# Optimization experiments

Measured on AMD Instinct MI355X. Metric: run time of the kernel, lower is better.

## Reference

```python
import jax, jax.numpy as jnp
import numpy as np

NUM_RELS = 1315
FEAT_DIM = 768
RD = 32  # rel_emb_dim
OD = 32  # out_dim
B = 65536  # entities per side
NNZ = 1048576  # nonzeros per incidence matrix (avg degree 16)
EPS = 1e-12  # torch F.normalize eps


def _normalize(x):
    n = jnp.linalg.norm(x, axis=1, keepdims=True)
    return x / jnp.maximum(n, EPS)


def _agg(rows, cols, vals, rel_emb):
    # sparse.mm(inc, rel_emb): gather rel rows, scale, scatter-add to entities -> [B, RD]
    return jax.ops.segment_sum(vals[:, None] * rel_emb[cols], rows, num_segments=B)


def _entity_emb(ri, ci, vi, ro, co, vo, feat, rel_emb, W_in, b_in, W_out, b_out, W_ent, b_ent):
    in_emb = _agg(ri, ci, vi, rel_emb) @ W_in.T + b_in
    out_emb = _agg(ro, co, vo, rel_emb) @ W_out.T + b_out
    f = jnp.concatenate([feat, in_emb, out_emb], axis=1)  # [B, FEAT+2*RD]
    return _normalize(f @ W_ent.T + b_ent)


def setup_inputs() -> dict:
    key = jax.random.key(0)
    ks = iter(jax.random.split(key, 40))
    d = {}
    for p in ("h", "pos_t", "neg_t"):
        for s in ("in", "out"):
            d[f"{p}_{s}_rows"] = jax.random.randint(next(ks), (NNZ,), 0, B, dtype=jnp.int32)
            d[f"{p}_{s}_cols"] = jax.random.randint(next(ks), (NNZ,), 0, NUM_RELS, dtype=jnp.int32)
            d[f"{p}_{s}_vals"] = jax.random.uniform(next(ks), (NNZ,), dtype=jnp.float32)
        d[f"{p}_node_feat"] = jax.random.normal(next(ks), (B, FEAT_DIM), dtype=jnp.float32)
    d["eid"] = jax.random.randint(next(ks), (B,), 0, NUM_RELS, dtype=jnp.int32)
    # learned parameters
    d["rel_emb"] = jax.random.normal(next(ks), (NUM_RELS, RD), dtype=jnp.float32) * 0.02
    d["W_in"] = jax.random.normal(next(ks), (RD, RD), dtype=jnp.float32) * 0.1
    d["b_in"] = jnp.zeros((RD,), dtype=jnp.float32)
    d["W_out"] = jax.random.normal(next(ks), (RD, RD), dtype=jnp.float32) * 0.1
    d["b_out"] = jnp.zeros((RD,), dtype=jnp.float32)
    d["W_ent"] = jax.random.normal(next(ks), (OD, FEAT_DIM + 2 * RD), dtype=jnp.float32) * 0.02
    d["b_ent"] = jnp.zeros((OD,), dtype=jnp.float32)
    d["W_rel"] = jax.random.normal(next(ks), (OD, RD), dtype=jnp.float32) * 0.1
    d["b_rel"] = jnp.zeros((OD,), dtype=jnp.float32)
    return d


def reference(h_in_rows, h_in_cols, h_in_vals, h_out_rows, h_out_cols, h_out_vals, h_node_feat,
              pos_t_in_rows, pos_t_in_cols, pos_t_in_vals, pos_t_out_rows, pos_t_out_cols, pos_t_out_vals, pos_t_node_feat,
              neg_t_in_rows, neg_t_in_cols, neg_t_in_vals, neg_t_out_rows, neg_t_out_cols, neg_t_out_vals, neg_t_node_feat,
              eid, rel_emb, W_in, b_in, W_out, b_out, W_ent, b_ent, W_rel, b_rel):
    r_emb = _normalize(rel_emb[eid] @ W_rel.T + b_rel)  # [B, OD]
    h_emb = _entity_emb(h_in_rows, h_in_cols, h_in_vals, h_out_rows, h_out_cols, h_out_vals,
                        h_node_feat, rel_emb, W_in, b_in, W_out, b_out, W_ent, b_ent)
    pos_t_emb = _entity_emb(pos_t_in_rows, pos_t_in_cols, pos_t_in_vals, pos_t_out_rows, pos_t_out_cols, pos_t_out_vals,
                            pos_t_node_feat, rel_emb, W_in, b_in, W_out, b_out, W_ent, b_ent)
    neg_t_emb = _entity_emb(neg_t_in_rows, neg_t_in_cols, neg_t_in_vals, neg_t_out_rows, neg_t_out_cols, neg_t_out_vals,
                            neg_t_node_feat, rel_emb, W_in, b_in, W_out, b_out, W_ent, b_ent)
    pos_score = jnp.linalg.norm(h_emb + r_emb - pos_t_emb, axis=1)
    neg_score = jnp.linalg.norm(h_emb + r_emb - neg_t_emb, axis=1)
    return (pos_score, neg_score)
```

## Files before the change

kernel.cpp:

```cpp
#include <hip/hip_runtime.h>
#include <math.h>

#define N_RELS 1315
#define NB 65536
#define NNZV (1 << 20)
#define FEATD 768

#define NBUK 256
#define CAP  4608
#define FPT  9

typedef float f32x4 __attribute__((ext_vector_type(4)));
typedef short s16x8 __attribute__((ext_vector_type(8)));
typedef float v2f  __attribute__((ext_vector_type(2)));

struct Mats { const int* rows[6]; const int* cols[6]; const float* vals[6]; };

__device__ __forceinline__ short f2bf(float f) {
    return __builtin_bit_cast(short, (__bf16)f);
}

__global__ void k_prep(const float* __restrict__ rel_emb,
                       const float* __restrict__ W_in, const float* __restrict__ b_in,
                       const float* __restrict__ W_out, const float* __restrict__ b_out,
                       const float* __restrict__ W_ent, const float* __restrict__ b_ent,
                       const float* __restrict__ W_rel, const float* __restrict__ b_rel,
                       float* __restrict__ Pcat, float* __restrict__ Prel,
                       float* __restrict__ bprime, unsigned* __restrict__ cursor)
{
    __shared__ float C[2][32][33];
    const int tid = threadIdx.x;
    if (cursor != nullptr && blockIdx.x < 6) {
        const int i = blockIdx.x * 256 + tid;
        cursor[i] = (unsigned)i * CAP;
    }
    for (int idx = tid; idx < 2 * 32 * 32; idx += 256) {
        int d = idx >> 10, o = (idx >> 5) & 31, t = idx & 31;
        const float* W  = d ? W_out : W_in;
        const float* we = W_ent + o * 832 + 768 + d * 32;
        float s = 0.f;
        #pragma unroll
        for (int j = 0; j < 32; ++j) s += we[j] * W[j * 32 + t];
        C[d][o][t] = s;
    }
    __syncthreads();

    const int row8 = blockIdx.x * 8 + (tid >> 5);
    const int o = tid & 31;
    if (row8 < 2 * N_RELS) {
        const int d = (row8 >= N_RELS) ? 1 : 0;
        const int r = row8 - d * N_RELS;
        const float* re = rel_emb + r * 32;
        float s = 0.f;
        #pragma unroll
        for (int t = 0; t < 32; ++t) s += re[t] * C[d][o][t];
        Pcat[row8 * 32 + o] = s;
    } else if (row8 < 3 * N_RELS) {
        const int r = row8 - 2 * N_RELS;
        const float* re = rel_emb + r * 32;
        float s = b_rel[o];
        #pragma unroll
        for (int j = 0; j < 32; ++j) s += W_rel[o * 32 + j] * re[j];
        float sq = s * s;
        #pragma unroll
        for (int m = 16; m; m >>= 1) sq += __shfl_xor(sq, m);
        Prel[r * 32 + o] = s / fmaxf(sqrtf(sq), 1e-12f);
    }
    if (blockIdx.x == 0 && tid < 32) {
        float s = b_ent[tid];
        #pragma unroll
        for (int j = 0; j < 32; ++j)
            s += b_in[j] * W_ent[tid * 832 + 768 + j] + b_out[j] * W_ent[tid * 832 + 800 + j];
        bprime[tid] = s;
    }
}

__global__ void k_wfrag(const float* __restrict__ W_ent, s16x8* __restrict__ wsB)
{
    const int t = blockIdx.x * 256 + threadIdx.x;
    if (t >= 24 * 2 * 64) return;
    const int kk = t >> 7, rem = t & 127, nt = rem >> 6, l = rem & 63;
    const int col = nt * 16 + (l & 15);
    const int k0  = kk * 32 + ((l >> 4) << 3);
    const float* w = W_ent + col * 832 + k0;
    s16x8 v;
    #pragma unroll
    for (int e = 0; e < 8; ++e) v[e] = f2bf(w[e]);
    wsB[t] = v;
}

__global__ __launch_bounds__(512) void k_bin(Mats m, uint2* __restrict__ bins,
                                             unsigned* __restrict__ cursor)
{
    __shared__ uint2 stage[4096];
    __shared__ int hist[256], sc[256], ofs[256];
    __shared__ unsigned gbase[256];
    const int bi    = blockIdx.x;
    const int mm    = bi >> 8;
    const int chunk = bi & 255;
    const int tid   = threadIdx.x;
    const int* __restrict__ R = m.rows[mm];
    const int* __restrict__ C = m.cols[mm];
    const float* __restrict__ V = m.vals[mm];
    const int base = chunk * 4096;

    if (tid < 256) hist[tid] = 0;
    __syncthreads();

    unsigned meta[8]; float val[8]; unsigned short lrank[8];
    #pragma unroll
    for (int e = 0; e < 8; ++e) {
        const int idx = base + e * 512 + tid;
        const int row = R[idx];
        const int col = C[idx];
        val[e]  = V[idx];
        meta[e] = ((unsigned)row << 11) | (unsigned)col;
        lrank[e] = (unsigned short)atomicAdd(&hist[meta[e] >> 19], 1);
    }
    __syncthreads();

    if (tid < 256) sc[tid] = hist[tid];
    __syncthreads();
    for (int off = 1; off < 256; off <<= 1) {
        const int x = (tid >= off && tid < 256) ? sc[tid - off] : 0;
        __syncthreads();
        if (tid < 256) sc[tid] += x;
        __syncthreads();
    }
    if (tid < 256) {
        ofs[tid]   = tid ? sc[tid - 1] : 0;
        gbase[tid] = atomicAdd(&cursor[mm * NBUK + tid], hist[tid]);
    }
    __syncthreads();

    #pragma unroll
    for (int e = 0; e < 8; ++e)
        stage[ofs[meta[e] >> 19] + lrank[e]] = make_uint2(meta[e], __float_as_uint(val[e]));
    __syncthreads();

    #pragma unroll
    for (int e = 0; e < 8; ++e) {
        const int i = e * 512 + tid;
        const uint2 ed = stage[i];
        const unsigned buk = ed.x >> 19;
        bins[gbase[buk] + (unsigned)(i - ofs[buk])] = make_uint2(ed.x & 0x7FFFFu, ed.y);
    }
}

__global__ __launch_bounds__(512) void k_fuse(const uint2* __restrict__ bins,
                                              const unsigned* __restrict__ cursor,
                                              const float* __restrict__ Pcat,
                                              float* __restrict__ aggY)
{
    __shared__ uint2 stage[CAP];
    __shared__ int hist[256], sc[256], ofs[256];
    const int set = blockIdx.x >> 8;
    const int b   = blockIdx.x & 255;
    const int t   = threadIdx.x;
    const int row  = t >> 1;
    const int half = t & 1;

    float acc[16];
    #pragma unroll
    for (int j = 0; j < 16; ++j) acc[j] = 0.f;

    for (int dir = 0; dir < 2; ++dir) {
        const int mb = (set * 2 + dir) * NBUK + b;
        const unsigned segbase = (unsigned)mb * CAP;
        const uint2* __restrict__ seg = bins + segbase;
        const int len = (int)(cursor[mb] - segbase);
        const float* __restrict__ P = Pcat + (size_t)dir * N_RELS * 32;

        if (t < 256) hist[t] = 0;
        __syncthreads();

        uint2 e[FPT];
        #pragma unroll
        for (int j = 0; j < FPT; ++j) {
            const int i = t + j * 512;
            if (i < len) e[j] = seg[i];
        }
        #pragma unroll
        for (int j = 0; j < FPT; ++j) {
            const int i = t + j * 512;
            if (i < len) atomicAdd(&hist[e[j].x >> 11], 1);
        }
        __syncthreads();

        if (t < 256) sc[t] = hist[t];
        __syncthreads();
        for (int off = 1; off < 256; off <<= 1) {
            const int x = (t >= off && t < 256) ? sc[t - off] : 0;
            __syncthreads();
            if (t < 256) sc[t] += x;
            __syncthreads();
        }
        if (t < 256) ofs[t] = t ? sc[t - 1] : 0;
        __syncthreads();
        const int myo = row ? sc[row - 1] : 0;
        const int myc = hist[row];

        #pragma unroll
        for (int j = 0; j < FPT; ++j) {
            const int i = t + j * 512;
            if (i < len) {
                const int pos = atomicAdd(&ofs[e[j].x >> 11], 1);
                stage[pos] = make_uint2(e[j].x & 2047u, e[j].y);
            }
        }
        __syncthreads();

        uint2 ed = (myc > 0) ? stage[myo] : make_uint2(0u, 0u);
        for (int j = 0; j < myc; ++j) {
            const uint2 nxt = (j + 1 < myc) ? stage[myo + j + 1] : make_uint2(0u, 0u);
            const float v = __uint_as_float(ed.y);
            const float4* prow = reinterpret_cast<const float4*>(P + (ed.x << 5) + half * 16);
            float4 p[4];
            #pragma unroll
            for (int q = 0; q < 4; ++q) p[q] = prow[q];
            #pragma unroll
            for (int q = 0; q < 4; ++q) {
                acc[q * 4 + 0] += v * p[q].x; acc[q * 4 + 1] += v * p[q].y;
                acc[q * 4 + 2] += v * p[q].z; acc[q * 4 + 3] += v * p[q].w;
            }
            ed = nxt;
        }
        __syncthreads();
    }

    float4* dst = reinterpret_cast<float4*>(
        aggY + ((size_t)set * NB + (size_t)b * 256 + row) * 32 + half * 16);
    #pragma unroll
    for (int q = 0; q < 4; ++q) {
        float4 wv;
        wv.x = acc[q * 4 + 0]; wv.y = acc[q * 4 + 1];
        wv.z = acc[q * 4 + 2]; wv.w = acc[q * 4 + 3];
        dst[q] = wv;
    }
}

__global__ void k_scatter(const int* __restrict__ rows, const int* __restrict__ cols,
                          const float* __restrict__ vals,
                          const float* __restrict__ Ptab, float* __restrict__ accs)
{
    const int stride = gridDim.x * blockDim.x;
    const int total = NNZV << 4;
    for (int g = blockIdx.x * blockDim.x + threadIdx.x; g < total; g += stride) {
        const int c2 = (g & 15) << 1;
        const int i  = g >> 4;
        const int row = rows[i];
        const int col = cols[i];
        const float v = vals[i];
        const float* p = Ptab + (col << 5) + c2;
        const int dst = (row << 5) + c2;
#if defined(__has_builtin) && __has_builtin(__builtin_amdgcn_global_atomic_fadd_v2f32)
        typedef __attribute__((address_space(1))) v2f* v2f_as1;
        v2f pv; pv.x = v * p[0]; pv.y = v * p[1];
        __builtin_amdgcn_global_atomic_fadd_v2f32(
            (v2f_as1)(unsigned long long)(accs + dst), pv);
#else
        atomicAdd(accs + dst,     v * p[0]);
        atomicAdd(accs + dst + 1, v * p[1]);
#endif
    }
}

__global__ __launch_bounds__(256) void k_gemm(
    const float* __restrict__ feat_h, const float* __restrict__ feat_p,
    const float* __restrict__ feat_n,
    const s16x8* __restrict__ wsB, const float* __restrict__ bprime,
    const float* __restrict__ aggY, const int* __restrict__ eid,
    const float* __restrict__ Prel, float* __restrict__ out)
{
    __shared__ f32x4 lA[2][64 * 17];
    __shared__ float lbp[32];

    const int tid  = threadIdx.x;
    const int lane = tid & 63;
    const int w    = tid >> 6;
    const int bid  = blockIdx.x;
    const int tile = (bid & 7) * 128 + (bid >> 3);
    const int e0   = tile << 6;

    const int l15 = lane & 15;
    const int kq  = lane >> 4;

    if (tid < 32) lbp[tid] = bprime[tid];

    const int srow = tid >> 4;
    const int scol = tid & 15;
    const s16x8* wsl = wsB + lane;
    const int rowA = (w << 4) + l15;

    f32x4 aH0 = {0.f,0.f,0.f,0.f}, aH1 = {0.f,0.f,0.f,0.f};
    f32x4 aP0 = {0.f,0.f,0.f,0.f}, aP1 = {0.f,0.f,0.f,0.f};
    f32x4 aN0 = {0.f,0.f,0.f,0.f}, aN1 = {0.f,0.f,0.f,0.f};

#define NTL(P) __builtin_nontemporal_load(P)

#define GEMM_SET(FEATP, A0, A1) do { \
    const f32x4* gs0 = reinterpret_cast<const f32x4*>((FEATP) + (size_t)(e0 + srow)      * FEATD) + scol; \
    const f32x4* gs1 = reinterpret_cast<const f32x4*>((FEATP) + (size_t)(e0 + 16 + srow) * FEATD) + scol; \
    const f32x4* gs2 = reinterpret_cast<const f32x4*>((FEATP) + (size_t)(e0 + 32 + srow) * FEATD) + scol; \
    const f32x4* gs3 = reinterpret_cast<const f32x4*>((FEATP) + (size_t)(e0 + 48 + srow) * FEATD) + scol; \
    f32x4 r0 = NTL(gs0), r1 = NTL(gs1), r2 = NTL(gs2), r3 = NTL(gs3); \
    lA[0][(srow     ) * 17 + scol] = r0; \
    lA[0][(srow + 16) * 17 + scol] = r1; \
    lA[0][(srow + 32) * 17 + scol] = r2; \
    lA[0][(srow + 48) * 17 + scol] = r3; \
    r0 = NTL(gs0 + 16); r1 = NTL(gs1 + 16); r2 = NTL(gs2 + 16); r3 = NTL(gs3 + 16); \
    __syncthreads(); \
    for (int c = 0; c < 12; ++c) { \
        if (c < 11) { \
            lA[(c + 1) & 1][(srow     ) * 17 + scol] = r0; \
            lA[(c + 1) & 1][(srow + 16) * 17 + scol] = r1; \
            lA[(c + 1) & 1][(srow + 32) * 17 + scol] = r2; \
            lA[(c + 1) & 1][(srow + 48) * 17 + scol] = r3; \
            if (c < 10) { \
                r0 = NTL(gs0 + (c + 2) * 16); r1 = NTL(gs1 + (c + 2) * 16); \
                r2 = NTL(gs2 + (c + 2) * 16); r3 = NTL(gs3 + (c + 2) * 16); \
            } \
        } \
        _Pragma("unroll") \
        for (int s = 0; s < 2; ++s) { \
            const int kk = c * 2 + s; \
            const f32x4 fa0 = lA[c & 1][rowA * 17 + s * 8 + kq * 2]; \
            const f32x4 fa1 = lA[c & 1][rowA * 17 + s * 8 + kq * 2 + 1]; \
            s16x8 av; \
            av[0] = f2bf(fa0.x); av[1] = f2bf(fa0.y); av[2] = f2bf(fa0.z); av[3] = f2bf(fa0.w); \
            av[4] = f2bf(fa1.x); av[5] = f2bf(fa1.y); av[6] = f2bf(fa1.z); av[7] = f2bf(fa1.w); \
            const s16x8 wb0 = wsl[(kk * 2 + 0) << 6]; \
            const s16x8 wb1 = wsl[(kk * 2 + 1) << 6]; \
            A0 = __builtin_amdgcn_mfma_f32_16x16x32_bf16(av, wb0, A0, 0, 0, 0); \
            A1 = __builtin_amdgcn_mfma_f32_16x16x32_bf16(av, wb1, A1, 0, 0, 0); \
        } \
        __syncthreads(); \
    } \
} while (0)

    GEMM_SET(feat_h, aH0, aH1);
    GEMM_SET(feat_p, aP0, aP1);
    GEMM_SET(feat_n, aN0, aN1);

#undef GEMM_SET
#undef NTL

    const float bp0 = lbp[l15], bp1 = lbp[l15 + 16];
    const int rbase = e0 + (w << 4) + (kq << 2);

#define NORM1(A0_, A1_, SOFF, Y0_, Y1_) do { \
    float v0 = (A0_)[e] + bp0 + aggY[(SOFF) + eoff + l15]; \
    float v1 = (A1_)[e] + bp1 + aggY[(SOFF) + eoff + l15 + 16]; \
    float sq = v0 * v0 + v1 * v1; \
    sq += __shfl_xor(sq, 1); sq += __shfl_xor(sq, 2); \
    sq += __shfl_xor(sq, 4); sq += __shfl_xor(sq, 8); \
    const float inv = 1.f / fmaxf(sqrtf(sq), 1e-12f); \
    Y0_ = v0 * inv; Y1_ = v1 * inv; \
} while (0)

    #pragma unroll
    for (int e = 0; e < 4; ++e) {
        const int ent = rbase + e;
        const size_t eoff = (size_t)ent * 32;
        float yh0, yh1, yp0, yp1, yn0, yn1;
        NORM1(aH0, aH1, (size_t)0,           yh0, yh1);
        NORM1(aP0, aP1, (size_t)NB * 32,     yp0, yp1);
        NORM1(aN0, aN1, (size_t)2 * NB * 32, yn0, yn1);
        const int ev = eid[ent];
        const float r0 = Prel[(size_t)ev * 32 + l15];
        const float r1 = Prel[(size_t)ev * 32 + l15 + 16];
        const float dp0 = yh0 + r0 - yp0, dp1 = yh1 + r1 - yp1;
        const float dn0 = yh0 + r0 - yn0, dn1 = yh1 + r1 - yn1;
        float sp = dp0 * dp0 + dp1 * dp1;
        float sn = dn0 * dn0 + dn1 * dn1;
        sp += __shfl_xor(sp, 1); sn += __shfl_xor(sn, 1);
        sp += __shfl_xor(sp, 2); sn += __shfl_xor(sn, 2);
        sp += __shfl_xor(sp, 4); sn += __shfl_xor(sn, 4);
        sp += __shfl_xor(sp, 8); sn += __shfl_xor(sn, 8);
        if (l15 == 0) { out[ent] = sqrtf(sp); out[NB + ent] = sqrtf(sn); }
    }
#undef NORM1
}

extern "C" void kernel_launch(void* const* d_in, const int* in_sizes, int n_in,
                              void* d_out, int out_size, void* d_ws, size_t ws_size,
                              hipStream_t stream)
{
    const float* feat_h = (const float*)d_in[6];
    const float* feat_p = (const float*)d_in[13];
    const float* feat_n = (const float*)d_in[20];
    const int*   eid    = (const int*)d_in[21];
    const float* rel_emb = (const float*)d_in[22];
    const float* W_in  = (const float*)d_in[23];
    const float* b_in  = (const float*)d_in[24];
    const float* W_out = (const float*)d_in[25];
    const float* b_out = (const float*)d_in[26];
    const float* W_ent = (const float*)d_in[27];
    const float* b_ent = (const float*)d_in[28];
    const float* W_rel = (const float*)d_in[29];
    const float* b_rel = (const float*)d_in[30];

    char* ws = (char*)d_ws;
    const size_t AGG_B   = (size_t)3 * NB * 32 * 4;
    const size_t BINS_B  = (size_t)6 * NBUK * CAP * 8;
    const size_t CURS_B  = 8192;
    const size_t PCAT_B  = (size_t)2 * N_RELS * 32 * 4;
    const size_t PREL_B  = (size_t)N_RELS * 32 * 4;
    const size_t BPR_B   = 128;
    const size_t WSB_B   = (size_t)24 * 2 * 64 * 16;
    const bool fast = ws_size >= AGG_B + BINS_B + CURS_B
                                + PCAT_B + PREL_B + BPR_B + WSB_B;

    float* aggY = (float*)ws;
    size_t off = AGG_B;
    uint2* bins = nullptr; unsigned* cursor = nullptr;
    if (fast) {
        bins   = (uint2*)(ws + off);    off += BINS_B;
        cursor = (unsigned*)(ws + off); off += CURS_B;
    }
    float* Pcat   = (float*)(ws + off); off += PCAT_B;
    float* Prel   = (float*)(ws + off); off += PREL_B;
    float* bprime = (float*)(ws + off); off += BPR_B;
    s16x8* wsB    = (s16x8*)(ws + off);

    k_prep<<<(3 * N_RELS + 7) / 8, 256, 0, stream>>>(rel_emb, W_in, b_in, W_out, b_out,
                                                     W_ent, b_ent, W_rel, b_rel,
                                                     Pcat, Prel, bprime, cursor);
    k_wfrag<<<12, 256, 0, stream>>>(W_ent, wsB);

    static const int base_idx[6] = {0, 3, 7, 10, 14, 17};
    if (fast) {
        Mats m;
        for (int i = 0; i < 6; ++i) {
            m.rows[i] = (const int*)d_in[base_idx[i]];
            m.cols[i] = (const int*)d_in[base_idx[i] + 1];
            m.vals[i] = (const float*)d_in[base_idx[i] + 2];
        }
        k_bin<<<6 * 256, 512, 0, stream>>>(m, bins, cursor);
        k_fuse<<<3 * 256, 512, 0, stream>>>(bins, cursor, Pcat, aggY);
    } else {
        hipMemsetAsync(aggY, 0, AGG_B, stream);
        for (int mm = 0; mm < 6; ++mm) {
            const int d = mm & 1, s = mm >> 1;
            k_scatter<<<32768, 256, 0, stream>>>((const int*)d_in[base_idx[mm]],
                                                 (const int*)d_in[base_idx[mm] + 1],
                                                 (const float*)d_in[base_idx[mm] + 2],
                                                 Pcat + (size_t)d * N_RELS * 32,
                                                 aggY + (size_t)s * NB * 32);
        }
    }

    k_gemm<<<1024, 256, 0, stream>>>(feat_h, feat_p, feat_n, wsB, bprime,
                                     aggY, eid, Prel, (float*)d_out);
}
```

Measured before the change: 232.8 us.

## Halve GEMM tile to 32 rows with 128-thread blocks, unroll fuse gather by two

The fused aggregation loop now handles two staged edges per iteration and issues both P-row loads together, replacing the one-edge software-prefetch chain, so more memory requests are in flight. The GEMM kernel moves from 64-row tiles with 256 threads to 32-row tiles with 128 threads and twice as many blocks, halving LDS per block to raise occupancy and spread work across more CUs. Smaller tiles reload the bf16 weight fragments more often per row, and the unseen epilogue must match the new row mapping.

```diff
diff --git a/kernel.cpp b/kernel.cpp
--- a/kernel.cpp
+++ b/kernel.cpp
@@ -210,20 +210,39 @@
         }
         __syncthreads();
 
-        uint2 ed = (myc > 0) ? stage[myo] : make_uint2(0u, 0u);
-        for (int j = 0; j < myc; ++j) {
-            const uint2 nxt = (j + 1 < myc) ? stage[myo + j + 1] : make_uint2(0u, 0u);
-            const float v = __uint_as_float(ed.y);
-            const float4* prow = reinterpret_cast<const float4*>(P + (ed.x << 5) + half * 16);
-            float4 p[4];
+        int j = 0;
+        for (; j + 2 <= myc; j += 2) {
+            const uint2 e0 = stage[myo + j];
+            const uint2 e1 = stage[myo + j + 1];
+            const float v0 = __uint_as_float(e0.y);
+            const float v1 = __uint_as_float(e1.y);
+            const float4* pr0 = reinterpret_cast<const float4*>(P + (e0.x << 5) + half * 16);
+            const float4* pr1 = reinterpret_cast<const float4*>(P + (e1.x << 5) + half * 16);
+            float4 p0[4], p1[4];
             #pragma unroll
-            for (int q = 0; q < 4; ++q) p[q] = prow[q];
+            for (int q = 0; q < 4; ++q) { p0[q] = pr0[q]; p1[q] = pr1[q]; }
             #pragma unroll
             for (int q = 0; q < 4; ++q) {
-                acc[q * 4 + 0] += v * p[q].x; acc[q * 4 + 1] += v * p[q].y;
-                acc[q * 4 + 2] += v * p[q].z; acc[q * 4 + 3] += v * p[q].w;
+                acc[q * 4 + 0] += v0 * p0[q].x + v1 * p1[q].x;
+                acc[q * 4 + 1] += v0 * p0[q].y + v1 * p1[q].y;
+                acc[q * 4 + 2] += v0 * p0[q].z + v1 * p1[q].z;
+                acc[q * 4 + 3] += v0 * p0[q].w + v1 * p1[q].w;
             }
-            ed = nxt;
+        }
+        if (j < myc) {
+            const uint2 e0 = stage[myo + j];
+            const float v0 = __uint_as_float(e0.y);
+            const float4* pr0 = reinterpret_cast<const float4*>(P + (e0.x << 5) + half * 16);
+            float4 p0[4];
+            #pragma unroll
+            for (int q = 0; q < 4; ++q) p0[q] = pr0[q];
+            #pragma unroll
+            for (int q = 0; q < 4; ++q) {
+                acc[q * 4 + 0] += v0 * p0[q].x;
+                acc[q * 4 + 1] += v0 * p0[q].y;
+                acc[q * 4 + 2] += v0 * p0[q].z;
+                acc[q * 4 + 3] += v0 * p0[q].w;
+            }
         }
         __syncthreads();
     }
@@ -265,22 +284,22 @@
     }
 }
 
-__global__ __launch_bounds__(256) void k_gemm(
+__global__ __launch_bounds__(128) void k_gemm(
     const float* __restrict__ feat_h, const float* __restrict__ feat_p,
     const float* __restrict__ feat_n,
     const s16x8* __restrict__ wsB, const float* __restrict__ bprime,
     const float* __restrict__ aggY, const int* __restrict__ eid,
     const float* __restrict__ Prel, float* __restrict__ out)
 {
-    __shared__ f32x4 lA[2][64 * 17];
+    __shared__ f32x4 lA[2][32 * 17];
     __shared__ float lbp[32];
 
     const int tid  = threadIdx.x;
     const int lane = tid & 63;
     const int w    = tid >> 6;
     const int bid  = blockIdx.x;
-    const int tile = (bid & 7) * 128 + (bid >> 3);
-    const int e0   = tile << 6;
+    const int tile = (bid & 7) * 256 + (bid >> 3);
+    const int e0   = tile << 5;
 
     const int l15 = lane & 15;
     const int kq  = lane >> 4;
@@ -300,22 +319,22 @@
 
 #define GEMM_SET(FEATP, A0, A1) do { \
     const f32x4* gs0 = reinterpret_cast<const f32x4*>((FEATP) + (size_t)(e0 + srow)      * FEATD) + scol; \
-    const f32x4* gs1 = reinterpret_cast<const f32x4*>((FEATP) + (size_t)(e0 + 16 + srow) * FEATD) + scol; \
-    const f32x4* gs2 = reinterpret_cast<const f32x4*>((FEATP) + (size_t)(e0 + 32 + srow) * FEATD) + scol; \
-    const f32x4* gs3 = reinterpret_cast<const f32x4*>((FEATP) + (size_t)(e0 + 48 + srow) * FEATD) + scol; \
+    const f32x4* gs1 = reinterpret_cast<const f32x4*>((FEATP) + (size_t)(e0 + 8  + srow) * FEATD) + scol; \
+    const f32x4* gs2 = reinterpret_cast<const f32x4*>((FEATP) + (size_t)(e0 + 16 + srow) * FEATD) + scol; \
+    const f32x4* gs3 = reinterpret_cast<const f32x4*>((FEATP) + (size_t)(e0 + 24 + srow) * FEATD) + scol; \
     f32x4 r0 = NTL(gs0), r1 = NTL(gs1), r2 = NTL(gs2), r3 = NTL(gs3); \
     lA[0][(srow     ) * 17 + scol] = r0; \
-    lA[0][(srow + 16) * 17 + scol] = r1; \
-    lA[0][(srow + 32) * 17 + scol] = r2; \
-    lA[0][(srow + 48) * 17 + scol] = r3; \
+    lA[0][(srow + 8 ) * 17 + scol] = r1; \
+    lA[0][(srow + 16) * 17 + scol] = r2; \
+    lA[0][(srow + 24) * 17 + scol] = r3; \
     r0 = NTL(gs0 + 16); r1 = NTL(gs1 + 16); r2 = NTL(gs2 + 16); r3 = NTL(gs3 + 16); \
     __syncthreads(); \
     for (int c = 0; c < 12; ++c) { \
         if (c < 11) { \
             lA[(c + 1) & 1][(srow     ) * 17 + scol] = r0; \
-            lA[(c + 1) & 1][(srow + 16) * 17 + scol] = r1; \
-            lA[(c + 1) & 1][(srow + 32) * 17 + scol] = r2; \
-            lA[(c + 1) & 1][(srow + 48) * 17 + scol] = r3; \
+            lA[(c + 1) & 1][(srow + 8 ) * 17 + scol] = r1; \
+            lA[(c + 1) & 1][(srow + 16) * 17 + scol] = r2; \
+            lA[(c + 1) & 1][(srow + 24) * 17 + scol] = r3; \
             if (c < 10) { \
                 r0 = NTL(gs0 + (c + 2) * 16); r1 = NTL(gs1 + (c + 2) * 16); \
                 r2 = NTL(gs2 + (c + 2) * 16); r3 = NTL(gs3 + (c + 2) * 16); \
@@ -450,6 +469,6 @@
         }
     }
 
-    k_gemm<<<1024, 256, 0, stream>>>(feat_h, feat_p, feat_n, wsB, bprime,
+    k_gemm<<<2048, 128, 0, stream>>>(feat_h, feat_p, feat_n, wsB, bprime,
                                      aggY, eid, Prel, (float*)d_out);
 }
```

After: 250.1 us. 1.07x slower.
